# Kernel optimization log

Hardware: AMD Instinct MI355X
Metric: run time of the kernel (lower is better)

The kernel has to match this reference:

```python
import jax, jax.numpy as jnp
import numpy as np

TEMPERATURE = 0.1
GAMMA = 0.5
LOSS_WEIGHT = 1.0
LINE_CLASS = 2
COS_EPS = 1e-8      # torch F.cosine_similarity eps
RADIUS = 1.0        # positive-pair spatial radius
SELF_EPS = 1e-6     # excludes self pairs (dist ~ 0) from positives
NCE_EPS = 1e-6


def _pairwise_dist(coords):
    # Euclidean cdist [N, N] with a sqrt that is safe at 0 (self pairs)
    sq = jnp.sum(coords * coords, axis=1)
    d2 = jnp.maximum(sq[:, None] + sq[None, :] - 2.0 * (coords @ coords.T), 0.0)
    safe = jnp.where(d2 > 0.0, d2, 1.0)
    return jnp.where(d2 > 0.0, jnp.sqrt(safe), 0.0)


def setup_inputs() -> dict:
    key = jax.random.key(0)
    k1, k2, k3 = jax.random.split(key, 3)
    N, D = 4096, 64
    features = jax.random.normal(k1, (N, D), dtype=jnp.float32)
    # uniform in a 10x10x10 box -> ~30 neighbors within radius 1.0 per point
    coords = jax.random.uniform(k2, (N, 3), dtype=jnp.float32) * 10.0
    labels = jax.random.randint(k3, (N,), 0, 3)  # class 2 == power line
    return {"features": features, "labels": labels, "coords": coords}


def reference(features, labels, coords):
    # Static-shape equivalent of boolean-indexing the line-class points:
    # weight w_i = 1 iff labels[i] == LINE_CLASS. All sums / means below are
    # restricted to line points via w, matching torch masked gather exactly.
    w = (labels == LINE_CLASS).astype(features.dtype)        # [N]
    M = jnp.sum(w)                                           # number of line points
    pair_w = w[:, None] * w[None, :]                         # [N, N]

    # cosine similarity matrix  [N, N]
    norms = jnp.maximum(jnp.linalg.norm(features, axis=1, keepdims=True), COS_EPS)
    fn = features / norms
    feat_sim = fn @ fn.T

    # spatial distance matrix and pos / neg pair masks  [N, N]
    coord_dist = _pairwise_dist(coords)
    pos_raw = ((coord_dist < RADIUS) & (coord_dist > SELF_EPS)).astype(features.dtype)
    pos_w = pair_w * pos_raw
    neg_w = pair_w * (1.0 - pos_raw)   # ~pos_mask within line subset (incl. self)

    # InfoNCE over line points
    exp_sim = jnp.exp(feat_sim / TEMPERATURE)
    pos_sum = jnp.sum(exp_sim * pos_w, axis=1)               # [N]
    neg_sum = jnp.sum(exp_sim * neg_w, axis=1)               # [N]
    ratio = pos_sum / (neg_sum + pos_sum + NCE_EPS)
    per_point = -jnp.log(jnp.where(w > 0, ratio, 1.0))       # 0 for non-line pts
    info_nce = jnp.sum(per_point) / M                        # mean over line pts

    # continuity: mean over the M x M line-pair block
    feat_dist = 1.0 - feat_sim
    continuity = jnp.sum(jnp.abs(feat_dist - coord_dist) * pos_w) / (M * M)

    return (info_nce + GAMMA * continuity) * LOSS_WEIGHT
```

## Files before the change

### kernel.cpp

```cpp
#include <hip/hip_runtime.h>
#include <hip/hip_bf16.h>

#define LINE_CLASS 2
#define NJ 12

__global__ __launch_bounds__(256) void compact_kernel(const int* __restrict__ labels,
                                                      int N, int* __restrict__ idx,
                                                      int* __restrict__ Mout) {
    __shared__ int wcnt[4];
    __shared__ int base;
    const int tid = threadIdx.x;
    if (tid == 0) base = 0;
    __syncthreads();
    for (int s = 0; s < N; s += 256) {
        const int i = s + tid;
        const bool p = (i < N) && (labels[i] == LINE_CLASS);
        const unsigned long long m = __ballot(p);
        const int wid = tid >> 6, lane = tid & 63;
        if (lane == 0) wcnt[wid] = __popcll(m);
        __syncthreads();
        int off = base;
        for (int w = 0; w < wid; ++w) off += wcnt[w];
        off += __popcll(m & ((1ull << lane) - 1ull));
        if (p) idx[off] = i;
        __syncthreads();
        if (tid == 0) base += wcnt[0] + wcnt[1] + wcnt[2] + wcnt[3];
        __syncthreads();
    }
    if (tid == 0) *Mout = base;
}

__global__ __launch_bounds__(64) void prep_kernel(const float* __restrict__ feat,
                                                  const float* __restrict__ coords,
                                                  const int* __restrict__ idx,
                                                  const int* __restrict__ Mp,
                                                  float* __restrict__ fnC,
                                                  float4* __restrict__ cC) {
    const int b = blockIdx.x;
    const int M = *Mp;
    if (b >= M) return;
    const int i = idx[b];
    const int d = threadIdx.x;
    const float v = feat[i * 64 + d];
    float ss = v * v;
    #pragma unroll
    for (int off = 32; off > 0; off >>= 1) ss += __shfl_xor(ss, off);
    const float nrm = sqrtf(ss);
    const float dn  = fmaxf(nrm, 1e-8f);
    fnC[b * 64 + d] = v / dn;
    if (d == 0) {
        const float x = coords[i * 3 + 0];
        const float y = coords[i * 3 + 1];
        const float z = coords[i * 3 + 2];
        const float sq = fmaf(x, x, fmaf(y, y, z * z));
        cC[b] = make_float4(x, y, z, sq);
    }
}

__global__ __launch_bounds__(256, 2) void pair_kernel(const float* __restrict__ fnC,
                                                      const float4* __restrict__ cC,
                                                      const int* __restrict__ Mp,
                                                      int N,
                                                      float* __restrict__ posp,
                                                      float* __restrict__ negp,
                                                      float* __restrict__ contp) {
    const int b  = blockIdx.x;
    const int js = blockIdx.y;
    const int tid = threadIdx.x;
    const int r = tid & 63;
    const int q = tid >> 6;
    const int M = *Mp;
    const int k = b * 64 + r;

    if (b * 64 >= M) {
        if (tid == 0) contp[b * NJ + js] = 0.0f;
        return;
    }
    const bool valid = (k < M);

    float f[64];
    if (valid) {
        #pragma unroll
        for (int d = 0; d < 64; ++d) f[d] = fnC[k * 64 + d];
    } else {
        #pragma unroll
        for (int d = 0; d < 64; ++d) f[d] = 0.0f;
    }
    const float4 ci = valid ? cC[k] : make_float4(0.f, 0.f, 0.f, 0.f);

    const int chunk = (M + NJ - 1) / NJ;
    const int j0 = js * chunk;
    const int j1 = (j0 + chunk < M) ? (j0 + chunk) : M;

    float pos = 0.0f, neg = 0.0f, cont = 0.0f;

    for (int j = j0 + q; j < j1; j += 4) {
        const int ju = __builtin_amdgcn_readfirstlane(j);
        const float* __restrict__ fj = fnC + (size_t)ju * 64;
        float dot = 0.0f;
        #pragma unroll
        for (int d = 0; d < 64; ++d) dot = fmaf(f[d], fj[d], dot);
        const float4 cj = cC[ju];
        const float cdot = fmaf(ci.x, cj.x, fmaf(ci.y, cj.y, ci.z * cj.z));
        float d2 = ci.w + cj.w - 2.0f * cdot;
        d2 = fmaxf(d2, 0.0f);
        const float dist = (d2 > 0.0f) ? sqrtf(d2) : 0.0f;
        const float e = expf(dot * 10.0f);
        const bool isPos = (dist < 1.0f) && (dist > 1e-6f);
        if (isPos) {
            pos += e;
            if (valid) cont += fabsf((1.0f - dot) - dist);
        } else {
            neg += e;
        }
    }

    __shared__ float sp[4][64];
    __shared__ float sn[4][64];
    __shared__ float sc[256];
    sp[q][r] = pos;
    sn[q][r] = neg;
    sc[tid] = cont;
    __syncthreads();
    if (q == 0) {
        const float P  = sp[0][r] + sp[1][r] + sp[2][r] + sp[3][r];
        const float Ng = sn[0][r] + sn[1][r] + sn[2][r] + sn[3][r];
        posp[js * N + k] = P;
        negp[js * N + k] = Ng;
    }
    for (int s = 128; s > 0; s >>= 1) {
        if (tid < s) sc[tid] += sc[tid + s];
        __syncthreads();
    }
    if (tid == 0) contp[b * NJ + js] = sc[0];
}

__global__ __launch_bounds__(1024) void final_kernel(const float* __restrict__ posp,
                                                     const float* __restrict__ negp,
                                                     const float* __restrict__ contp,
                                                     const int* __restrict__ Mp,
                                                     int N, int NB,
                                                     float* __restrict__ out) {
    const int tid = threadIdx.x;
    const int M = *Mp;
    float nce = 0.0f;
    for (int k = tid; k < M; k += 1024) {
        float P = 0.0f, Ng = 0.0f;
        for (int js = 0; js < NJ; ++js) {
            P  += posp[js * N + k];
            Ng += negp[js * N + k];
        }
        const float ratio = fmaxf(P / (Ng + P + 1e-6f), 1e-38f);
        nce += -logf(ratio);
    }
    float cont = 0.0f;
    const int nslots = NB * NJ;
    for (int c = tid; c < nslots; c += 1024) cont += contp[c];

    __shared__ float r1[1024];
    __shared__ float r2[1024];
    r1[tid] = nce;
    r2[tid] = cont;
    __syncthreads();
    for (int s = 512; s > 0; s >>= 1) {
        if (tid < s) { r1[tid] += r1[tid + s]; r2[tid] += r2[tid + s]; }
        __syncthreads();
    }
    if (tid == 0) {
        const float Mf = (float)M;
        const float info_nce   = r1[0] / Mf;
        const float continuity = r2[0] / (Mf * Mf);
        out[0] = (info_nce + 0.5f * continuity) * 1.0f;
    }
}

extern "C" void kernel_launch(void* const* d_in, const int* in_sizes, int n_in,
                              void* d_out, int out_size, void* d_ws, size_t ws_size,
                              hipStream_t stream) {
    const float* feat   = (const float*)d_in[0];
    const int*   labels = (const int*)  d_in[1];
    const float* coords = (const float*)d_in[2];
    const int N = in_sizes[1];

    char* ws = (char*)d_ws;
    int*    Mp   = (int*)   (ws + 0);
    int*    idx  = (int*)   (ws + 1024);
    float4* cC   = (float4*)(ws + 32768);
    float*  fnC  = (float*) (ws + 131072);
    float*  posp = (float*) (ws + 131072 + (size_t)256 * N);
    float*  negp = (float*) (ws + 131072 + (size_t)256 * N + (size_t)4 * NJ * N);
    float*  contp= (float*) (ws + 131072 + (size_t)256 * N + (size_t)8 * NJ * N);

    const int NB = (N + 63) / 64;

    compact_kernel<<<1, 256, 0, stream>>>(labels, N, idx, Mp);
    prep_kernel<<<N, 64, 0, stream>>>(feat, coords, idx, Mp, fnC, cC);
    pair_kernel<<<dim3(NB, NJ), 256, 0, stream>>>(fnC, cC, Mp, N, posp, negp, contp);
    final_kernel<<<1, 1024, 0, stream>>>(posp, negp, contp, Mp, N, NB, (float*)d_out);
}
```

Measured before the change: 103.9 us.

## Fuse final reduction into pair kernel via last-block counter and raise split count

Drops the separate final kernel: each pair block bumps an atomic counter, and the last block to finish does the InfoNCE and continuity reduction. The j-split count rises from 12 to 32 to give more blocks, and the per-row partials move to a row-major layout so the final pass reads them as float4. The compact kernel now uses 1024 threads and also builds the coordinate table, and the prep kernel packs four rows per block. This saves one launch and improves occupancy, but adds a serial tail reduction in a single 256-thread block and relies on fence/atomic ordering for correctness.

```diff
diff --git a/kernel.cpp b/kernel.cpp
--- a/kernel.cpp
+++ b/kernel.cpp
@@ -2,21 +2,24 @@
 #include <hip/hip_bf16.h>
 
 #define LINE_CLASS 2
-#define NJ 12
-
-__global__ __launch_bounds__(256) void compact_kernel(const int* __restrict__ labels,
-                                                      int N, int* __restrict__ idx,
-                                                      int* __restrict__ Mout) {
-    __shared__ int wcnt[4];
+#define NJ 32
+
+__global__ __launch_bounds__(1024) void compact_kernel(const int* __restrict__ labels,
+                                                       const float* __restrict__ coords,
+                                                       int N, int* __restrict__ idx,
+                                                       int* __restrict__ Mout,
+                                                       int* __restrict__ counter,
+                                                       float4* __restrict__ cC) {
+    __shared__ int wcnt[16];
     __shared__ int base;
     const int tid = threadIdx.x;
+    const int wid = tid >> 6, lane = tid & 63;
     if (tid == 0) base = 0;
     __syncthreads();
-    for (int s = 0; s < N; s += 256) {
+    for (int s = 0; s < N; s += 1024) {
         const int i = s + tid;
         const bool p = (i < N) && (labels[i] == LINE_CLASS);
         const unsigned long long m = __ballot(p);
-        const int wid = tid >> 6, lane = tid & 63;
         if (lane == 0) wcnt[wid] = __popcll(m);
         __syncthreads();
         int off = base;
@@ -24,46 +27,50 @@
         off += __popcll(m & ((1ull << lane) - 1ull));
         if (p) idx[off] = i;
         __syncthreads();
-        if (tid == 0) base += wcnt[0] + wcnt[1] + wcnt[2] + wcnt[3];
-        __syncthreads();
-    }
-    if (tid == 0) *Mout = base;
-}
-
-__global__ __launch_bounds__(64) void prep_kernel(const float* __restrict__ feat,
-                                                  const float* __restrict__ coords,
-                                                  const int* __restrict__ idx,
-                                                  const int* __restrict__ Mp,
-                                                  float* __restrict__ fnC,
-                                                  float4* __restrict__ cC) {
-    const int b = blockIdx.x;
-    const int M = *Mp;
-    if (b >= M) return;
-    const int i = idx[b];
-    const int d = threadIdx.x;
-    const float v = feat[i * 64 + d];
-    float ss = v * v;
-    #pragma unroll
-    for (int off = 32; off > 0; off >>= 1) ss += __shfl_xor(ss, off);
-    const float nrm = sqrtf(ss);
-    const float dn  = fmaxf(nrm, 1e-8f);
-    fnC[b * 64 + d] = v / dn;
-    if (d == 0) {
+        if (tid == 0) {
+            int t = 0;
+            for (int w = 0; w < 16; ++w) t += wcnt[w];
+            base += t;
+        }
+        __syncthreads();
+    }
+    const int M = base;
+    for (int b = tid; b < M; b += 1024) {
+        const int i = idx[b];
         const float x = coords[i * 3 + 0];
         const float y = coords[i * 3 + 1];
         const float z = coords[i * 3 + 2];
         const float sq = fmaf(x, x, fmaf(y, y, z * z));
         cC[b] = make_float4(x, y, z, sq);
     }
+    if (tid == 0) { *Mout = M; *counter = 0; }
+}
+
+__global__ __launch_bounds__(256) void prep_kernel(const float* __restrict__ feat,
+                                                   const int* __restrict__ idx,
+                                                   const int* __restrict__ Mp,
+                                                   float* __restrict__ fnC) {
+    const int b = blockIdx.x * 4 + (threadIdx.x >> 6);
+    const int d = threadIdx.x & 63;
+    const int M = *Mp;
+    if (b >= M) return;
+    const int i = idx[b];
+    const float v = feat[i * 64 + d];
+    float ss = v * v;
+    #pragma unroll
+    for (int off = 32; off > 0; off >>= 1) ss += __shfl_xor(ss, off);
+    const float dn = fmaxf(sqrtf(ss), 1e-8f);
+    fnC[b * 64 + d] = v / dn;
 }
 
 __global__ __launch_bounds__(256, 2) void pair_kernel(const float* __restrict__ fnC,
                                                       const float4* __restrict__ cC,
                                                       const int* __restrict__ Mp,
-                                                      int N,
+                                                      int* __restrict__ counter,
                                                       float* __restrict__ posp,
                                                       float* __restrict__ negp,
-                                                      float* __restrict__ contp) {
+                                                      float* __restrict__ contp,
+                                                      float* __restrict__ out) {
     const int b  = blockIdx.x;
     const int js = blockIdx.y;
     const int tid = threadIdx.x;
@@ -71,106 +78,119 @@
     const int q = tid >> 6;
     const int M = *Mp;
     const int k = b * 64 + r;
-
-    if (b * 64 >= M) {
-        if (tid == 0) contp[b * NJ + js] = 0.0f;
-        return;
-    }
-    const bool valid = (k < M);
-
-    float f[64];
-    if (valid) {
-        #pragma unroll
-        for (int d = 0; d < 64; ++d) f[d] = fnC[k * 64 + d];
-    } else {
-        #pragma unroll
-        for (int d = 0; d < 64; ++d) f[d] = 0.0f;
-    }
-    const float4 ci = valid ? cC[k] : make_float4(0.f, 0.f, 0.f, 0.f);
-
-    const int chunk = (M + NJ - 1) / NJ;
-    const int j0 = js * chunk;
-    const int j1 = (j0 + chunk < M) ? (j0 + chunk) : M;
-
-    float pos = 0.0f, neg = 0.0f, cont = 0.0f;
-
-    for (int j = j0 + q; j < j1; j += 4) {
-        const int ju = __builtin_amdgcn_readfirstlane(j);
-        const float* __restrict__ fj = fnC + (size_t)ju * 64;
-        float dot = 0.0f;
-        #pragma unroll
-        for (int d = 0; d < 64; ++d) dot = fmaf(f[d], fj[d], dot);
-        const float4 cj = cC[ju];
-        const float cdot = fmaf(ci.x, cj.x, fmaf(ci.y, cj.y, ci.z * cj.z));
-        float d2 = ci.w + cj.w - 2.0f * cdot;
-        d2 = fmaxf(d2, 0.0f);
-        const float dist = (d2 > 0.0f) ? sqrtf(d2) : 0.0f;
-        const float e = expf(dot * 10.0f);
-        const bool isPos = (dist < 1.0f) && (dist > 1e-6f);
-        if (isPos) {
-            pos += e;
-            if (valid) cont += fabsf((1.0f - dot) - dist);
-        } else {
-            neg += e;
-        }
-    }
+    const bool active = (b * 64 < M);
 
     __shared__ float sp[4][64];
     __shared__ float sn[4][64];
     __shared__ float sc[256];
-    sp[q][r] = pos;
-    sn[q][r] = neg;
-    sc[tid] = cont;
-    __syncthreads();
-    if (q == 0) {
-        const float P  = sp[0][r] + sp[1][r] + sp[2][r] + sp[3][r];
-        const float Ng = sn[0][r] + sn[1][r] + sn[2][r] + sn[3][r];
-        posp[js * N + k] = P;
-        negp[js * N + k] = Ng;
-    }
-    for (int s = 128; s > 0; s >>= 1) {
-        if (tid < s) sc[tid] += sc[tid + s];
-        __syncthreads();
-    }
-    if (tid == 0) contp[b * NJ + js] = sc[0];
-}
-
-__global__ __launch_bounds__(1024) void final_kernel(const float* __restrict__ posp,
-                                                     const float* __restrict__ negp,
-                                                     const float* __restrict__ contp,
-                                                     const int* __restrict__ Mp,
-                                                     int N, int NB,
-                                                     float* __restrict__ out) {
-    const int tid = threadIdx.x;
-    const int M = *Mp;
+    __shared__ int lastflag;
+
+    if (active) {
+        const bool valid = (k < M);
+        float4 f4[16];
+        if (valid) {
+            const float4* fr = (const float4*)(fnC + (size_t)k * 64);
+            #pragma unroll
+            for (int t = 0; t < 16; ++t) f4[t] = fr[t];
+        } else {
+            #pragma unroll
+            for (int t = 0; t < 16; ++t) f4[t] = make_float4(0.f, 0.f, 0.f, 0.f);
+        }
+        const float4 ci = valid ? cC[k] : make_float4(0.f, 0.f, 0.f, 0.f);
+
+        const int chunk = (M + NJ - 1) / NJ;
+        const int j0 = js * chunk;
+        const int j1 = (j0 + chunk < M) ? (j0 + chunk) : M;
+
+        float pos = 0.0f, neg = 0.0f, cont = 0.0f;
+        for (int j = j0 + q; j < j1; j += 4) {
+            const int ju = __builtin_amdgcn_readfirstlane(j);
+            const float4* __restrict__ fjv = (const float4*)(fnC + (size_t)ju * 64);
+            float dot = 0.0f;
+            #pragma unroll
+            for (int t = 0; t < 16; ++t) {
+                const float4 bv = fjv[t];
+                dot = fmaf(f4[t].x, bv.x, dot);
+                dot = fmaf(f4[t].y, bv.y, dot);
+                dot = fmaf(f4[t].z, bv.z, dot);
+                dot = fmaf(f4[t].w, bv.w, dot);
+            }
+            const float4 cj = cC[ju];
+            const float cdot = fmaf(ci.x, cj.x, fmaf(ci.y, cj.y, ci.z * cj.z));
+            float d2 = fmaxf(ci.w + cj.w - 2.0f * cdot, 0.0f);
+            const float dist = (d2 > 0.0f) ? sqrtf(d2) : 0.0f;
+            const float e = expf(dot * 10.0f);
+            const bool isPos = (dist < 1.0f) && (dist > 1e-6f);
+            if (isPos) {
+                pos += e;
+                if (valid) cont += fabsf((1.0f - dot) - dist);
+            } else {
+                neg += e;
+            }
+        }
+
+        sp[q][r] = pos;
+        sn[q][r] = neg;
+        sc[tid] = cont;
+        __syncthreads();
+        if (q == 0) {
+            posp[(size_t)k * NJ + js] = sp[0][r] + sp[1][r] + sp[2][r] + sp[3][r];
+            negp[(size_t)k * NJ + js] = sn[0][r] + sn[1][r] + sn[2][r] + sn[3][r];
+        }
+        for (int s = 128; s > 0; s >>= 1) {
+            if (tid < s) sc[tid] += sc[tid + s];
+            __syncthreads();
+        }
+        if (tid == 0) contp[b * NJ + js] = sc[0];
+    } else {
+        if (tid == 0) contp[b * NJ + js] = 0.0f;
+    }
+
+    __threadfence();
+    __syncthreads();
+    if (tid == 0) {
+        const int total = (int)(gridDim.x * gridDim.y);
+        const int prev = __hip_atomic_fetch_add(counter, 1, __ATOMIC_ACQ_REL,
+                                                __HIP_MEMORY_SCOPE_AGENT);
+        lastflag = (prev == total - 1) ? 1 : 0;
+    }
+    __syncthreads();
+    if (!lastflag) return;
+    __threadfence();
+
     float nce = 0.0f;
-    for (int k = tid; k < M; k += 1024) {
+    for (int kk = tid; kk < M; kk += 256) {
+        const float4* pv = (const float4*)(posp + (size_t)kk * NJ);
+        const float4* nv = (const float4*)(negp + (size_t)kk * NJ);
         float P = 0.0f, Ng = 0.0f;
-        for (int js = 0; js < NJ; ++js) {
-            P  += posp[js * N + k];
-            Ng += negp[js * N + k];
+        #pragma unroll
+        for (int t = 0; t < NJ / 4; ++t) {
+            const float4 a = pv[t];
+            P += a.x + a.y + a.z + a.w;
+            const float4 g = nv[t];
+            Ng += g.x + g.y + g.z + g.w;
         }
         const float ratio = fmaxf(P / (Ng + P + 1e-6f), 1e-38f);
         nce += -logf(ratio);
     }
     float cont = 0.0f;
-    const int nslots = NB * NJ;
-    for (int c = tid; c < nslots; c += 1024) cont += contp[c];
-
-    __shared__ float r1[1024];
-    __shared__ float r2[1024];
+    const int nslots = (int)gridDim.x * NJ;
+    for (int c = tid; c < nslots; c += 256) cont += contp[c];
+
+    sp[0][0] = 0.0f;
+    __syncthreads();
+    float* r1 = &sp[0][0];
+    float* r2 = &sc[0];
     r1[tid] = nce;
     r2[tid] = cont;
     __syncthreads();
-    for (int s = 512; s > 0; s >>= 1) {
+    for (int s = 128; s > 0; s >>= 1) {
         if (tid < s) { r1[tid] += r1[tid + s]; r2[tid] += r2[tid + s]; }
         __syncthreads();
     }
     if (tid == 0) {
         const float Mf = (float)M;
-        const float info_nce   = r1[0] / Mf;
-        const float continuity = r2[0] / (Mf * Mf);
-        out[0] = (info_nce + 0.5f * continuity) * 1.0f;
+        out[0] = (r1[0] / Mf + 0.5f * (r2[0] / (Mf * Mf))) * 1.0f;
     }
 }
 
@@ -183,18 +203,19 @@
     const int N = in_sizes[1];
 
     char* ws = (char*)d_ws;
-    int*    Mp   = (int*)   (ws + 0);
-    int*    idx  = (int*)   (ws + 1024);
-    float4* cC   = (float4*)(ws + 32768);
-    float*  fnC  = (float*) (ws + 131072);
-    float*  posp = (float*) (ws + 131072 + (size_t)256 * N);
-    float*  negp = (float*) (ws + 131072 + (size_t)256 * N + (size_t)4 * NJ * N);
-    float*  contp= (float*) (ws + 131072 + (size_t)256 * N + (size_t)8 * NJ * N);
+    int*    Mp      = (int*)   (ws + 0);
+    int*    counter = (int*)   (ws + 64);
+    int*    idx     = (int*)   (ws + 1024);
+    float4* cC      = (float4*)(ws + 32768);
+    float*  fnC     = (float*) (ws + 131072);
+    float*  posp    = (float*) (ws + 2097152);
+    float*  negp    = (float*) (ws + 2621440);
+    float*  contp   = (float*) (ws + 3145728);
 
     const int NB = (N + 63) / 64;
 
-    compact_kernel<<<1, 256, 0, stream>>>(labels, N, idx, Mp);
-    prep_kernel<<<N, 64, 0, stream>>>(feat, coords, idx, Mp, fnC, cC);
-    pair_kernel<<<dim3(NB, NJ), 256, 0, stream>>>(fnC, cC, Mp, N, posp, negp, contp);
-    final_kernel<<<1, 1024, 0, stream>>>(posp, negp, contp, Mp, N, NB, (float*)d_out);
-}
+    compact_kernel<<<1, 1024, 0, stream>>>(labels, coords, N, idx, Mp, counter, cC);
+    prep_kernel<<<(N + 3) / 4, 256, 0, stream>>>(feat, idx, Mp, fnC);
+    pair_kernel<<<dim3(NB, NJ), 256, 0, stream>>>(fnC, cC, Mp, counter,
+                                                  posp, negp, contp, (float*)d_out);
+}
```

Result: slower. 285.4 us (+174.7%).
